# Performance work log

Measured on AMD Instinct MI355X. Metric: run time of the kernel, lower is better.

The kernel has to match this reference:

```python
import jax, jax.numpy as jnp
import numpy as np

N_NODES = 50000
N_EDGES = 1600000
EDGE_DIM = 64
NODE_DIM = 128
GLOBAL_DIM = 64
IN_DIM = EDGE_DIM + NODE_DIM + GLOBAL_DIM  # 256
HID_DIM = 256
OUT_DIM = 128


def setup_inputs() -> dict:
    key = jax.random.key(0)
    ks = jax.random.split(key, 8)
    edges = jax.random.normal(ks[0], (N_EDGES, EDGE_DIM), dtype=jnp.float32)
    receivers = jax.random.randint(ks[1], (N_EDGES,), 0, N_NODES, dtype=jnp.int64)
    nodes = jax.random.normal(ks[2], (N_NODES, NODE_DIM), dtype=jnp.float32)
    globals_ = jax.random.normal(ks[3], (1, GLOBAL_DIM), dtype=jnp.float32)
    # MLP params (Linear -> ReLU -> Linear), fan-in scaled init
    W1 = jax.random.normal(ks[4], (IN_DIM, HID_DIM), dtype=jnp.float32) / np.sqrt(IN_DIM)
    b1 = jnp.zeros((HID_DIM,), dtype=jnp.float32)
    W2 = jax.random.normal(ks[5], (HID_DIM, OUT_DIM), dtype=jnp.float32) / np.sqrt(HID_DIM)
    b2 = jnp.zeros((OUT_DIM,), dtype=jnp.float32)
    return {
        "edges": edges, "receivers": receivers, "nodes": nodes,
        "globals_": globals_, "num_nodes": N_NODES,
        "W1": W1, "b1": b1, "W2": W2, "b2": b2,
    }


def reference(edges, receivers, nodes, globals_, num_nodes, W1, b1, W2, b2):
    # ReceivedEdgesToNodesAggregator: unsorted_segment_sum of edge features to receiver nodes
    agg = jax.ops.segment_sum(edges, receivers, num_segments=num_nodes)  # [N, EDGE_DIM]
    # broadcast_globals_to_nodes (single graph -> tile to every node)
    g = jnp.broadcast_to(globals_, (num_nodes, globals_.shape[-1]))      # [N, GLOBAL_DIM]
    collected = jnp.concatenate([agg, nodes, g], axis=-1)                # [N, IN_DIM]
    h = jax.nn.relu(collected @ W1 + b1)
    updated_nodes = h @ W2 + b2                                          # [N, OUT_DIM]
    return updated_nodes
```

## Files before the change

### kernel.cpp

```cpp
#include <hip/hip_runtime.h>


typedef __bf16 bf16x8 __attribute__((ext_vector_type(8)));
typedef __bf16 bf16x4 __attribute__((ext_vector_type(4)));
typedef __bf16 bf16x2 __attribute__((ext_vector_type(2)));
typedef float f32x4 __attribute__((ext_vector_type(4)));
typedef int i32x4 __attribute__((ext_vector_type(4)));

#define EDGE_DIM 64
#define NODE_DIM 128
#define IN_DIM 256
#define HID_DIM 256
#define OUT_DIM 128
#define NBUCKET 512
#define NPB 98
#define EPB 4096
#define MT 64
#define HPAD 280

__global__ __launch_bounds__(256) void prep_hist_kernel(
    const float* __restrict__ W1, const float* __restrict__ W2,
    __bf16* __restrict__ W1T, __bf16* __restrict__ W2T,
    const int* __restrict__ recv, int* __restrict__ bh, int n_edges) {
  const int b = blockIdx.x, t = threadIdx.x;
  if (b < HID_DIM) { W1T[b * IN_DIM + t] = (__bf16)W1[t * HID_DIM + b]; return; }
  if (b < HID_DIM + OUT_DIM) {
    int nn = b - HID_DIM;
    W2T[nn * HID_DIM + t] = (__bf16)W2[t * OUT_DIM + nn];
    return;
  }
  const int hb = b - (HID_DIM + OUT_DIM);
  __shared__ int h[NBUCKET];
  for (int k = t; k < NBUCKET; k += 256) h[k] = 0;
  __syncthreads();
  const int i0 = hb * EPB + t * 16;
  if (i0 + 16 <= n_edges) {
#pragma unroll
    for (int c = 0; c < 4; ++c) {
      i32x4 r4 = *(const i32x4*)(recv + i0 + c * 4);
      atomicAdd(&h[r4.x / NPB], 1);
      atomicAdd(&h[r4.y / NPB], 1);
      atomicAdd(&h[r4.z / NPB], 1);
      atomicAdd(&h[r4.w / NPB], 1);
    }
  } else {
    for (int j = 0; j < 16; ++j)
      if (i0 + j < n_edges) atomicAdd(&h[recv[i0 + j] / NPB], 1);
  }
  __syncthreads();
  for (int k = t; k < NBUCKET; k += 256) bh[(size_t)hb * NBUCKET + k] = h[k];
}

__global__ __launch_bounds__(256) void col_scan_kernel(
    int* __restrict__ bh, int* __restrict__ tot, int nbh) {
  const int bucket = (blockIdx.x * 256 + threadIdx.x) >> 6;
  const int lane = threadIdx.x & 63;
  int running = 0;
  for (int c = 0; c < nbh; c += 64) {
    const int k = c + lane;
    int v = (k < nbh) ? bh[(size_t)k * NBUCKET + bucket] : 0;
    int incl = v;
    for (int off = 1; off < 64; off <<= 1) {
      int y = __shfl_up(incl, off, 64);
      if (lane >= off) incl += y;
    }
    if (k < nbh) bh[(size_t)k * NBUCKET + bucket] = running + incl - v;
    running += __shfl(incl, 63, 64);
  }
  if (lane == 0) tot[bucket] = running;
}

__global__ __launch_bounds__(512) void base_scan_kernel(const int* __restrict__ tot,
                                                        int* __restrict__ base) {
  const int b = threadIdx.x;
  int v = tot[b];
  __shared__ int sums[NBUCKET];
  sums[b] = v;
  __syncthreads();
  for (int off = 1; off < NBUCKET; off <<= 1) {
    int y = (b >= off) ? sums[b - off] : 0;
    __syncthreads();
    sums[b] += y;
    __syncthreads();
  }
  base[b] = sums[b] - v;
  if (b == NBUCKET - 1) base[NBUCKET] = sums[b];
}

__global__ __launch_bounds__(256) void scatter_kernel(
    const int* __restrict__ recv, const int* __restrict__ off,
    const int* __restrict__ base, int* __restrict__ sorted1, int n_edges) {
  const int kb = blockIdx.x, t = threadIdx.x;
  __shared__ int cur[NBUCKET];
  for (int k = t; k < NBUCKET; k += 256)
    cur[k] = base[k] + off[(size_t)kb * NBUCKET + k];
  __syncthreads();
  const int i0 = kb * EPB + t * 16;
  if (i0 + 16 <= n_edges) {
#pragma unroll
    for (int c = 0; c < 4; ++c) {
      i32x4 r4 = *(const i32x4*)(recv + i0 + c * 4);
      const int e0 = i0 + c * 4;
      int bk, p;
      bk = r4.x / NPB; p = atomicAdd(&cur[bk], 1);
      sorted1[p] = ((e0 + 0) << 7) | (r4.x - bk * NPB);
      bk = r4.y / NPB; p = atomicAdd(&cur[bk], 1);
      sorted1[p] = ((e0 + 1) << 7) | (r4.y - bk * NPB);
      bk = r4.z / NPB; p = atomicAdd(&cur[bk], 1);
      sorted1[p] = ((e0 + 2) << 7) | (r4.z - bk * NPB);
      bk = r4.w / NPB; p = atomicAdd(&cur[bk], 1);
      sorted1[p] = ((e0 + 3) << 7) | (r4.w - bk * NPB);
    }
  } else {
    for (int j = 0; j < 16; ++j) {
      const int i = i0 + j;
      if (i < n_edges) {
        int r = recv[i];
        int bk = r / NPB;
        int p = atomicAdd(&cur[bk], 1);
        sorted1[p] = (i << 7) | (r - bk * NPB);
      }
    }
  }
}

__global__ __launch_bounds__(256) void regroup_kernel(
    const int* __restrict__ sorted1, const int* __restrict__ base,
    int* __restrict__ nodeoff, int* __restrict__ ncount,
    int* __restrict__ eidcsr, int n_nodes) {
  const int b = blockIdx.x, t = threadIdx.x;
  __shared__ int cnt[NPB];
  __shared__ int loff[NPB];
  if (t < NPB) cnt[t] = 0;
  __syncthreads();
  const int s = base[b], e = base[b + 1];
  const int nb_ = b * NPB;
  for (int j = s + t; j < e; j += 256) atomicAdd(&cnt[sorted1[j] & 127], 1);
  __syncthreads();
  if (t == 0) {
    int run = 0;
#pragma unroll
    for (int k = 0; k < NPB; ++k) { loff[k] = run; run += cnt[k]; }
  }
  __syncthreads();
  if (t < NPB) {
    const int node = nb_ + t;
    if (node < n_nodes) { nodeoff[node] = s + loff[t]; ncount[node] = cnt[t]; }
    cnt[t] = 0;
  }
  __syncthreads();
  for (int j = s + t; j < e; j += 256) {
    const int p = sorted1[j];
    const int local = p & 127;
    const int slot = atomicAdd(&cnt[local], 1);
    eidcsr[s + loff[local] + slot] = p >> 7;
  }
}

__global__ __launch_bounds__(256) void build_x_kernel(
    const float* __restrict__ edges, const int* __restrict__ nodeoff,
    const int* __restrict__ ncount, const int* __restrict__ eid,
    const float* __restrict__ nodes, const float* __restrict__ glob,
    __bf16* __restrict__ X, int n_nodes) {
  const int gwave = (blockIdx.x * 256 + threadIdx.x) >> 6;
  const int lane = threadIdx.x & 63;
  if (gwave >= n_nodes) return;
  const int q = lane >> 4;
  const int l15 = lane & 15;
  const int s = nodeoff[gwave];
  const int e = s + ncount[gwave];
  f32x4 a0 = {0.f, 0.f, 0.f, 0.f}, a1 = a0, a2 = a0, a3 = a0;

  int j = s + q;
  int i0 = (j < e) ? eid[j] : 0;
  int i1 = (j + 4 < e) ? eid[j + 4] : 0;
  int i2 = (j + 8 < e) ? eid[j + 8] : 0;
  int i3 = (j + 12 < e) ? eid[j + 12] : 0;

  while (j + 12 < e) {
    f32x4 v0 = __builtin_nontemporal_load((const f32x4*)(edges + (size_t)i0 * EDGE_DIM + l15 * 4));
    f32x4 v1 = __builtin_nontemporal_load((const f32x4*)(edges + (size_t)i1 * EDGE_DIM + l15 * 4));
    f32x4 v2 = __builtin_nontemporal_load((const f32x4*)(edges + (size_t)i2 * EDGE_DIM + l15 * 4));
    f32x4 v3 = __builtin_nontemporal_load((const f32x4*)(edges + (size_t)i3 * EDGE_DIM + l15 * 4));
    int n0 = (j + 16 < e) ? eid[j + 16] : 0;
    int n1 = (j + 20 < e) ? eid[j + 20] : 0;
    int n2 = (j + 24 < e) ? eid[j + 24] : 0;
    int n3 = (j + 28 < e) ? eid[j + 28] : 0;
    a0 += v0; a1 += v1; a2 += v2; a3 += v3;
    i0 = n0; i1 = n1; i2 = n2; i3 = n3;
    j += 16;
  }
  if (j < e)
    a0 += __builtin_nontemporal_load((const f32x4*)(edges + (size_t)i0 * EDGE_DIM + l15 * 4));
  if (j + 4 < e)
    a1 += __builtin_nontemporal_load((const f32x4*)(edges + (size_t)i1 * EDGE_DIM + l15 * 4));
  if (j + 8 < e)
    a2 += __builtin_nontemporal_load((const f32x4*)(edges + (size_t)i2 * EDGE_DIM + l15 * 4));

  a0 += a1; a2 += a3; a0 += a2;
#pragma unroll
  for (int c = 0; c < 4; ++c) {
    float v = a0[c];
    v += __shfl_xor(v, 16, 64);
    v += __shfl_xor(v, 32, 64);
    a0[c] = v;
  }
  __bf16* row = X + (size_t)gwave * IN_DIM;
  if (q == 0) {
    bf16x4 o;
    o[0] = (__bf16)a0[0]; o[1] = (__bf16)a0[1];
    o[2] = (__bf16)a0[2]; o[3] = (__bf16)a0[3];
    *(bf16x4*)(row + l15 * 4) = o;
  }
  float2 nv = *(const float2*)(nodes + (size_t)gwave * NODE_DIM + lane * 2);
  bf16x2 nb;
  nb[0] = (__bf16)nv.x; nb[1] = (__bf16)nv.y;
  *(bf16x2*)(row + EDGE_DIM + lane * 2) = nb;
  if (lane < 32) {
    float2 gv = *(const float2*)(glob + lane * 2);
    bf16x2 gb;
    gb[0] = (__bf16)gv.x; gb[1] = (__bf16)gv.y;
    *(bf16x2*)(row + EDGE_DIM + NODE_DIM + lane * 2) = gb;
  }
}

__global__ __launch_bounds__(256, 2) void mlp_kernel(
    const __bf16* __restrict__ X, const __bf16* __restrict__ W1T,
    const float* __restrict__ b1, const __bf16* __restrict__ W2T,
    const float* __restrict__ b2, float* __restrict__ out, int M) {
  __shared__ __bf16 Hs[MT][HPAD];
  const int wave = threadIdx.x >> 6;
  const int lane = threadIdx.x & 63;
  const int l15 = lane & 15;
  const int lk = lane >> 4;
  const int Mbase0 = blockIdx.x * MT;

  {
    bf16x8 B1[4][8];
    float bias1[4];
    const int colbase = wave * 64;
#pragma unroll
    for (int cb = 0; cb < 4; ++cb) {
      const int col = colbase + cb * 16 + l15;
      const __bf16* wrow = W1T + col * IN_DIM + lk * 8;
#pragma unroll
      for (int ks = 0; ks < 8; ++ks) B1[cb][ks] = *(const bf16x8*)(wrow + ks * 32);
      bias1[cb] = b1[col];
    }
#pragma unroll
    for (int mb = 0; mb < 4; ++mb) {
      const int Mbase = Mbase0 + mb * 16;
      f32x4 acc[4];
#pragma unroll
      for (int cb = 0; cb < 4; ++cb) {
        f32x4 ini = {bias1[cb], bias1[cb], bias1[cb], bias1[cb]};
        acc[cb] = ini;
      }
      const __bf16* xrow = X + (size_t)(Mbase + l15) * IN_DIM + lk * 8;
#pragma unroll
      for (int ks = 0; ks < 8; ++ks) {
        bf16x8 A = *(const bf16x8*)(xrow + ks * 32);
#pragma unroll
        for (int cb = 0; cb < 4; ++cb)
          acc[cb] = __builtin_amdgcn_mfma_f32_16x16x32_bf16(A, B1[cb][ks], acc[cb], 0, 0, 0);
      }
#pragma unroll
      for (int cb = 0; cb < 4; ++cb) {
#pragma unroll
        for (int r = 0; r < 4; ++r) {
          float v = acc[cb][r];
          Hs[mb * 16 + lk * 4 + r][colbase + cb * 16 + l15] = (__bf16)(v > 0.f ? v : 0.f);
        }
      }
    }
  }
  __syncthreads();
  {
    bf16x8 B2[2][8];
    float bias2[2];
    const int colbase = wave * 32;
#pragma unroll
    for (int cb = 0; cb < 2; ++cb) {
      const int col = colbase + cb * 16 + l15;
      const __bf16* wrow = W2T + col * HID_DIM + lk * 8;
#pragma unroll
      for (int ks = 0; ks < 8; ++ks) B2[cb][ks] = *(const bf16x8*)(wrow + ks * 32);
      bias2[cb] = b2[col];
    }
#pragma unroll
    for (int mb = 0; mb < 4; ++mb) {
      const int Mbase = Mbase0 + mb * 16;
      f32x4 acc[2];
#pragma unroll
      for (int cb = 0; cb < 2; ++cb) {
        f32x4 ini = {bias2[cb], bias2[cb], bias2[cb], bias2[cb]};
        acc[cb] = ini;
      }
#pragma unroll
      for (int ks = 0; ks < 8; ++ks) {
        bf16x8 A = *(const bf16x8*)(&Hs[mb * 16 + l15][lk * 8 + ks * 32]);
#pragma unroll
        for (int cb = 0; cb < 2; ++cb)
          acc[cb] = __builtin_amdgcn_mfma_f32_16x16x32_bf16(A, B2[cb][ks], acc[cb], 0, 0, 0);
      }
#pragma unroll
      for (int cb = 0; cb < 2; ++cb) {
        const int col = colbase + cb * 16 + l15;
#pragma unroll
        for (int r = 0; r < 4; ++r) {
          const int row = Mbase + lk * 4 + r;
          if (row < M) out[(size_t)row * OUT_DIM + col] = acc[cb][r];
        }
      }
    }
  }
}

extern "C" void kernel_launch(void* const* d_in, const int* in_sizes, int n_in,
                              void* d_out, int out_size, void* d_ws, size_t ws_size,
                              hipStream_t stream) {
  const float* edges    = (const float*)d_in[0];
  const int*   recv     = (const int*)d_in[1];
  const float* nodes    = (const float*)d_in[2];
  const float* globals_ = (const float*)d_in[3];
  const float* W1       = (const float*)d_in[5];
  const float* b1       = (const float*)d_in[6];
  const float* W2       = (const float*)d_in[7];
  const float* b2       = (const float*)d_in[8];

  const int n_edges = in_sizes[0] / EDGE_DIM;
  const int n_nodes = in_sizes[2] / NODE_DIM;
  const int NBH = (n_edges + EPB - 1) / EPB;
  float* out = (float*)d_out;

  char* ws = (char*)d_ws;
  size_t off = 0;
  int* bh = (int*)(ws + off);      off += (size_t)NBH * NBUCKET * 4;
  off = (off + 255) & ~(size_t)255;
  int* tot = (int*)(ws + off);     off += NBUCKET * 4;
  off = (off + 255) & ~(size_t)255;
  int* base = (int*)(ws + off);    off += (NBUCKET + 1) * 4;
  off = (off + 255) & ~(size_t)255;
  int* sorted1 = (int*)(ws + off); off += (size_t)n_edges * 4;
  off = (off + 255) & ~(size_t)255;
  int* nodeoff = (int*)(ws + off); off += (size_t)n_nodes * 4;
  off = (off + 255) & ~(size_t)255;
  int* ncount = (int*)(ws + off);  off += (size_t)n_nodes * 4;
  off = (off + 255) & ~(size_t)255;
  int* eidcsr = (int*)(ws + off);  off += (size_t)n_edges * 4;
  off = (off + 255) & ~(size_t)255;
  __bf16* X   = (__bf16*)(ws + off); off += (size_t)n_nodes * IN_DIM * 2;
  __bf16* W1T = (__bf16*)(ws + off); off += (size_t)IN_DIM * HID_DIM * 2;
  __bf16* W2T = (__bf16*)(ws + off); off += (size_t)HID_DIM * OUT_DIM * 2;

  prep_hist_kernel<<<HID_DIM + OUT_DIM + NBH, 256, 0, stream>>>(W1, W2, W1T, W2T,
                                                                recv, bh, n_edges);
  col_scan_kernel<<<NBUCKET / 4, 256, 0, stream>>>(bh, tot, NBH);
  base_scan_kernel<<<1, NBUCKET, 0, stream>>>(tot, base);
  scatter_kernel<<<NBH, 256, 0, stream>>>(recv, bh, base, sorted1, n_edges);
  regroup_kernel<<<NBUCKET, 256, 0, stream>>>(sorted1, base, nodeoff, ncount,
                                              eidcsr, n_nodes);
  build_x_kernel<<<(n_nodes + 3) / 4, 256, 0, stream>>>(edges, nodeoff, ncount, eidcsr,
                                                        nodes, globals_, X, n_nodes);
  mlp_kernel<<<(n_nodes + MT - 1) / MT, 256, 0, stream>>>(X, W1T, b1, W2T, b2, out, n_nodes);
}
```

Measured before the change: 168.2 us.

## Fuse gather-aggregate into MLP kernel and fold globals into first-layer bias

The per-node edge aggregation and node-feature load now happen inside the MLP kernel and write a 64-row tile to shared memory. This removes the global X round trip and one kernel launch. The broadcast globals contribution to layer 1 is folded into an effective bias during weight prep, which shrinks the GEMM K dimension from 256 to 192. The edge gather loop is unrolled to 8 outstanding loads per wave. In exchange, each block now runs the gather phase before the MMA phase with no overlap between them. The extra shared-memory tile may also lower occupancy.

```diff
diff --git a/kernel.cpp b/kernel.cpp
--- a/kernel.cpp
+++ b/kernel.cpp
@@ -9,7 +9,8 @@
 
 #define EDGE_DIM 64
 #define NODE_DIM 128
-#define IN_DIM 256
+#define XDIM 192
+#define XPAD 200
 #define HID_DIM 256
 #define OUT_DIM 128
 #define NBUCKET 512
@@ -19,11 +20,21 @@
 #define HPAD 280
 
 __global__ __launch_bounds__(256) void prep_hist_kernel(
-    const float* __restrict__ W1, const float* __restrict__ W2,
-    __bf16* __restrict__ W1T, __bf16* __restrict__ W2T,
+    const float* __restrict__ W1, const float* __restrict__ b1,
+    const float* __restrict__ W2, const float* __restrict__ glob,
+    __bf16* __restrict__ W1T, float* __restrict__ b1f, __bf16* __restrict__ W2T,
     const int* __restrict__ recv, int* __restrict__ bh, int n_edges) {
   const int b = blockIdx.x, t = threadIdx.x;
-  if (b < HID_DIM) { W1T[b * IN_DIM + t] = (__bf16)W1[t * HID_DIM + b]; return; }
+  if (b < HID_DIM) {
+    if (t < XDIM) {
+      W1T[b * XDIM + t] = (__bf16)W1[t * HID_DIM + b];
+    } else {
+      float p = glob[t - XDIM] * W1[t * HID_DIM + b];
+      for (int off = 32; off; off >>= 1) p += __shfl_xor(p, off, 64);
+      if (t == XDIM) b1f[b] = b1[b] + p;
+    }
+    return;
+  }
   if (b < HID_DIM + OUT_DIM) {
     int nn = b - HID_DIM;
     W2T[nn * HID_DIM + t] = (__bf16)W2[t * OUT_DIM + nn];
@@ -157,108 +168,119 @@
   }
 }
 
-__global__ __launch_bounds__(256) void build_x_kernel(
+#define NTLOAD(i) __builtin_nontemporal_load((const f32x4*)(edges + (size_t)(i) * EDGE_DIM + l15 * 4))
+
+__global__ __launch_bounds__(256, 2) void fused_kernel(
     const float* __restrict__ edges, const int* __restrict__ nodeoff,
     const int* __restrict__ ncount, const int* __restrict__ eid,
-    const float* __restrict__ nodes, const float* __restrict__ glob,
-    __bf16* __restrict__ X, int n_nodes) {
-  const int gwave = (blockIdx.x * 256 + threadIdx.x) >> 6;
-  const int lane = threadIdx.x & 63;
-  if (gwave >= n_nodes) return;
-  const int q = lane >> 4;
-  const int l15 = lane & 15;
-  const int s = nodeoff[gwave];
-  const int e = s + ncount[gwave];
-  f32x4 a0 = {0.f, 0.f, 0.f, 0.f}, a1 = a0, a2 = a0, a3 = a0;
-
-  int j = s + q;
-  int i0 = (j < e) ? eid[j] : 0;
-  int i1 = (j + 4 < e) ? eid[j + 4] : 0;
-  int i2 = (j + 8 < e) ? eid[j + 8] : 0;
-  int i3 = (j + 12 < e) ? eid[j + 12] : 0;
-
-  while (j + 12 < e) {
-    f32x4 v0 = __builtin_nontemporal_load((const f32x4*)(edges + (size_t)i0 * EDGE_DIM + l15 * 4));
-    f32x4 v1 = __builtin_nontemporal_load((const f32x4*)(edges + (size_t)i1 * EDGE_DIM + l15 * 4));
-    f32x4 v2 = __builtin_nontemporal_load((const f32x4*)(edges + (size_t)i2 * EDGE_DIM + l15 * 4));
-    f32x4 v3 = __builtin_nontemporal_load((const f32x4*)(edges + (size_t)i3 * EDGE_DIM + l15 * 4));
-    int n0 = (j + 16 < e) ? eid[j + 16] : 0;
-    int n1 = (j + 20 < e) ? eid[j + 20] : 0;
-    int n2 = (j + 24 < e) ? eid[j + 24] : 0;
-    int n3 = (j + 28 < e) ? eid[j + 28] : 0;
-    a0 += v0; a1 += v1; a2 += v2; a3 += v3;
-    i0 = n0; i1 = n1; i2 = n2; i3 = n3;
-    j += 16;
-  }
-  if (j < e)
-    a0 += __builtin_nontemporal_load((const f32x4*)(edges + (size_t)i0 * EDGE_DIM + l15 * 4));
-  if (j + 4 < e)
-    a1 += __builtin_nontemporal_load((const f32x4*)(edges + (size_t)i1 * EDGE_DIM + l15 * 4));
-  if (j + 8 < e)
-    a2 += __builtin_nontemporal_load((const f32x4*)(edges + (size_t)i2 * EDGE_DIM + l15 * 4));
-
-  a0 += a1; a2 += a3; a0 += a2;
-#pragma unroll
-  for (int c = 0; c < 4; ++c) {
-    float v = a0[c];
-    v += __shfl_xor(v, 16, 64);
-    v += __shfl_xor(v, 32, 64);
-    a0[c] = v;
-  }
-  __bf16* row = X + (size_t)gwave * IN_DIM;
-  if (q == 0) {
-    bf16x4 o;
-    o[0] = (__bf16)a0[0]; o[1] = (__bf16)a0[1];
-    o[2] = (__bf16)a0[2]; o[3] = (__bf16)a0[3];
-    *(bf16x4*)(row + l15 * 4) = o;
-  }
-  float2 nv = *(const float2*)(nodes + (size_t)gwave * NODE_DIM + lane * 2);
-  bf16x2 nb;
-  nb[0] = (__bf16)nv.x; nb[1] = (__bf16)nv.y;
-  *(bf16x2*)(row + EDGE_DIM + lane * 2) = nb;
-  if (lane < 32) {
-    float2 gv = *(const float2*)(glob + lane * 2);
-    bf16x2 gb;
-    gb[0] = (__bf16)gv.x; gb[1] = (__bf16)gv.y;
-    *(bf16x2*)(row + EDGE_DIM + NODE_DIM + lane * 2) = gb;
-  }
-}
-
-__global__ __launch_bounds__(256, 2) void mlp_kernel(
-    const __bf16* __restrict__ X, const __bf16* __restrict__ W1T,
-    const float* __restrict__ b1, const __bf16* __restrict__ W2T,
-    const float* __restrict__ b2, float* __restrict__ out, int M) {
+    const float* __restrict__ nodes,
+    const __bf16* __restrict__ W1T, const float* __restrict__ b1f,
+    const __bf16* __restrict__ W2T, const float* __restrict__ b2,
+    float* __restrict__ out, int M) {
+  __shared__ __bf16 Xs[MT][XPAD];
   __shared__ __bf16 Hs[MT][HPAD];
   const int wave = threadIdx.x >> 6;
   const int lane = threadIdx.x & 63;
+  const int q = lane >> 4;
   const int l15 = lane & 15;
-  const int lk = lane >> 4;
+  const int lk = q;
   const int Mbase0 = blockIdx.x * MT;
 
+  for (int r = wave * 16; r < wave * 16 + 16; ++r) {
+    const int node = Mbase0 + r;
+    int s = 0, e = 0;
+    if (node < M) { s = nodeoff[node]; e = s + ncount[node]; }
+    f32x4 z = {0.f, 0.f, 0.f, 0.f};
+    f32x4 a0 = z, a1 = z, a2 = z, a3 = z, a4 = z, a5 = z, a6 = z, a7 = z;
+    int j = s + q;
+    int i0 = (j      < e) ? eid[j]      : 0;
+    int i1 = (j + 4  < e) ? eid[j + 4]  : 0;
+    int i2 = (j + 8  < e) ? eid[j + 8]  : 0;
+    int i3 = (j + 12 < e) ? eid[j + 12] : 0;
+    int i4 = (j + 16 < e) ? eid[j + 16] : 0;
+    int i5 = (j + 20 < e) ? eid[j + 20] : 0;
+    int i6 = (j + 24 < e) ? eid[j + 24] : 0;
+    int i7 = (j + 28 < e) ? eid[j + 28] : 0;
+    while (j + 28 < e) {
+      f32x4 v0 = NTLOAD(i0);
+      f32x4 v1 = NTLOAD(i1);
+      f32x4 v2 = NTLOAD(i2);
+      f32x4 v3 = NTLOAD(i3);
+      f32x4 v4 = NTLOAD(i4);
+      f32x4 v5 = NTLOAD(i5);
+      f32x4 v6 = NTLOAD(i6);
+      f32x4 v7 = NTLOAD(i7);
+      int n0 = (j + 32 < e) ? eid[j + 32] : 0;
+      int n1 = (j + 36 < e) ? eid[j + 36] : 0;
+      int n2 = (j + 40 < e) ? eid[j + 40] : 0;
+      int n3 = (j + 44 < e) ? eid[j + 44] : 0;
+      int n4 = (j + 48 < e) ? eid[j + 48] : 0;
+      int n5 = (j + 52 < e) ? eid[j + 52] : 0;
+      int n6 = (j + 56 < e) ? eid[j + 56] : 0;
+      int n7 = (j + 60 < e) ? eid[j + 60] : 0;
+      a0 += v0; a1 += v1; a2 += v2; a3 += v3;
+      a4 += v4; a5 += v5; a6 += v6; a7 += v7;
+      i0 = n0; i1 = n1; i2 = n2; i3 = n3;
+      i4 = n4; i5 = n5; i6 = n6; i7 = n7;
+      j += 32;
+    }
+    if (j      < e) a0 += NTLOAD(i0);
+    if (j + 4  < e) a1 += NTLOAD(i1);
+    if (j + 8  < e) a2 += NTLOAD(i2);
+    if (j + 12 < e) a3 += NTLOAD(i3);
+    if (j + 16 < e) a4 += NTLOAD(i4);
+    if (j + 20 < e) a5 += NTLOAD(i5);
+    if (j + 24 < e) a6 += NTLOAD(i6);
+
+    a0 += a1; a2 += a3; a4 += a5; a6 += a7;
+    a0 += a2; a4 += a6; a0 += a4;
+#pragma unroll
+    for (int c = 0; c < 4; ++c) {
+      float v = a0[c];
+      v += __shfl_xor(v, 16, 64);
+      v += __shfl_xor(v, 32, 64);
+      a0[c] = v;
+    }
+    if (q == 0) {
+      bf16x4 o;
+      o[0] = (__bf16)a0[0]; o[1] = (__bf16)a0[1];
+      o[2] = (__bf16)a0[2]; o[3] = (__bf16)a0[3];
+      *(bf16x4*)(&Xs[r][l15 * 4]) = o;
+    }
+    bf16x2 nb;
+    if (node < M) {
+      float2 nv = *(const float2*)(nodes + (size_t)node * NODE_DIM + lane * 2);
+      nb[0] = (__bf16)nv.x; nb[1] = (__bf16)nv.y;
+    } else {
+      nb[0] = (__bf16)0.f; nb[1] = (__bf16)0.f;
+    }
+    *(bf16x2*)(&Xs[r][EDGE_DIM + lane * 2]) = nb;
+  }
+  __syncthreads();
+
   {
-    bf16x8 B1[4][8];
+    bf16x8 B1[4][6];
     float bias1[4];
     const int colbase = wave * 64;
 #pragma unroll
     for (int cb = 0; cb < 4; ++cb) {
       const int col = colbase + cb * 16 + l15;
-      const __bf16* wrow = W1T + col * IN_DIM + lk * 8;
-#pragma unroll
-      for (int ks = 0; ks < 8; ++ks) B1[cb][ks] = *(const bf16x8*)(wrow + ks * 32);
-      bias1[cb] = b1[col];
+      const __bf16* wrow = W1T + col * XDIM + lk * 8;
+#pragma unroll
+      for (int ks = 0; ks < 6; ++ks) B1[cb][ks] = *(const bf16x8*)(wrow + ks * 32);
+      bias1[cb] = b1f[col];
     }
 #pragma unroll
     for (int mb = 0; mb < 4; ++mb) {
-      const int Mbase = Mbase0 + mb * 16;
       f32x4 acc[4];
 #pragma unroll
       for (int cb = 0; cb < 4; ++cb) {
         f32x4 ini = {bias1[cb], bias1[cb], bias1[cb], bias1[cb]};
         acc[cb] = ini;
       }
-      const __bf16* xrow = X + (size_t)(Mbase + l15) * IN_DIM + lk * 8;
-#pragma unroll
-      for (int ks = 0; ks < 8; ++ks) {
+      const __bf16* xrow = &Xs[mb * 16 + l15][lk * 8];
+#pragma unroll
+      for (int ks = 0; ks < 6; ++ks) {
         bf16x8 A = *(const bf16x8*)(xrow + ks * 32);
 #pragma unroll
         for (int cb = 0; cb < 4; ++cb)
@@ -349,18 +371,19 @@
   off = (off + 255) & ~(size_t)255;
   int* eidcsr = (int*)(ws + off);  off += (size_t)n_edges * 4;
   off = (off + 255) & ~(size_t)255;
-  __bf16* X   = (__bf16*)(ws + off); off += (size_t)n_nodes * IN_DIM * 2;
-  __bf16* W1T = (__bf16*)(ws + off); off += (size_t)IN_DIM * HID_DIM * 2;
+  __bf16* W1T = (__bf16*)(ws + off); off += (size_t)HID_DIM * XDIM * 2;
+  off = (off + 255) & ~(size_t)255;
+  float* b1f = (float*)(ws + off);  off += HID_DIM * 4;
+  off = (off + 255) & ~(size_t)255;
   __bf16* W2T = (__bf16*)(ws + off); off += (size_t)HID_DIM * OUT_DIM * 2;
 
-  prep_hist_kernel<<<HID_DIM + OUT_DIM + NBH, 256, 0, stream>>>(W1, W2, W1T, W2T,
-                                                                recv, bh, n_edges);
+  prep_hist_kernel<<<HID_DIM + OUT_DIM + NBH, 256, 0, stream>>>(
+      W1, b1, W2, globals_, W1T, b1f, W2T, recv, bh, n_edges);
   col_scan_kernel<<<NBUCKET / 4, 256, 0, stream>>>(bh, tot, NBH);
   base_scan_kernel<<<1, NBUCKET, 0, stream>>>(tot, base);
   scatter_kernel<<<NBH, 256, 0, stream>>>(recv, bh, base, sorted1, n_edges);
   regroup_kernel<<<NBUCKET, 256, 0, stream>>>(sorted1, base, nodeoff, ncount,
                                               eidcsr, n_nodes);
-  build_x_kernel<<<(n_nodes + 3) / 4, 256, 0, stream>>>(edges, nodeoff, ncount, eidcsr,
-                                                        nodes, globals_, X, n_nodes);
-  mlp_kernel<<<(n_nodes + MT - 1) / MT, 256, 0, stream>>>(X, W1T, b1, W2T, b2, out, n_nodes);
-}
+  fused_kernel<<<(n_nodes + MT - 1) / MT, 256, 0, stream>>>(
+      edges, nodeoff, ncount, eidcsr, nodes, W1T, b1f, W2T, b2, out, n_nodes);
+}
```

Measured after the change: 225.4 us. 34.0% more time.
